# Kernel optimization log

Measured on AMD Instinct MI355X. Metric: run time of the kernel, lower is better.

Reference implementation:

```python
import jax, jax.numpy as jnp
import numpy as np

N, E, DIN, DH, NG, DOUT = 65536, 524288, 128, 128, 256, 3
EPS = 1e-5  # torch BatchNorm1d default


def setup_inputs():
    key = jax.random.key(0)
    ks = jax.random.split(key, 32)

    def p(k, shape, s=0.05):
        return jax.random.normal(k, shape, jnp.float32) * s

    inp = {
        "x": jax.random.normal(ks[0], (N, DIN), jnp.float32),
        "edge_index": jax.random.randint(ks[1], (2, E), 0, N),
        "batch": jnp.sort(jax.random.randint(ks[2], (N,), 0, NG)),
    }
    # live GATv2 layers: gat1 128->128, gat2 128->64, gat3 64->32 (gat4 output is
    # overwritten by h4 = dropout(h3) in the source, so gat4/m4 are dead code)
    dims = [(DIN, 128), (128, 64), (64, 32)]
    i = 3
    for l, (di, do) in enumerate(dims, start=1):
        inp[f"g{l}_Wl"] = p(ks[i], (di, do)); i += 1
        inp[f"g{l}_bl"] = jnp.zeros((do,), jnp.float32)
        inp[f"g{l}_Wr"] = p(ks[i], (di, do)); i += 1
        inp[f"g{l}_br"] = jnp.zeros((do,), jnp.float32)
        inp[f"g{l}_att"] = p(ks[i], (do,)); i += 1
        inp[f"g{l}_b"] = jnp.zeros((do,), jnp.float32)
        inp[f"bn{l}_g"] = jnp.ones((do,), jnp.float32)
        inp[f"bn{l}_b"] = jnp.zeros((do,), jnp.float32)
    inp["lin1_W"] = p(ks[i], (256, 128)); i += 1
    inp["lin1_b"] = jnp.zeros((128,), jnp.float32)
    inp["bn5_g"] = jnp.ones((128,), jnp.float32)
    inp["bn5_b"] = jnp.zeros((128,), jnp.float32)
    inp["lin2_W"] = p(ks[i], (128, DOUT)); i += 1
    inp["lin2_b"] = jnp.zeros((DOUT,), jnp.float32)
    inp["train"] = 0  # dropout disabled (eval)
    return inp


def _bn(h, g, b):
    # BatchNorm1d with batch statistics (biased variance, as torch normalizes)
    mu = h.mean(0)
    var = h.var(0)
    return g * (h - mu) * jax.lax.rsqrt(var + EPS) + b


def _gatv2(x, src, dst, Wl, bl, Wr, br, att, b, n):
    xl = x @ Wl + bl  # [N, C] source-side transform (also the message value)
    xr = x @ Wr + br  # [N, C] target-side transform
    e = jax.nn.leaky_relu(xl[src] + xr[dst], 0.2) @ att  # [E] attention logits
    m = jax.ops.segment_max(e, dst, num_segments=n)      # segment softmax over in-edges
    ex = jnp.exp(e - m[dst])
    alpha = ex / jax.ops.segment_sum(ex, dst, num_segments=n)[dst]
    return jax.ops.segment_sum(alpha[:, None] * xl[src], dst, num_segments=n) + b


def reference(x, edge_index, batch,
              g1_Wl, g1_bl, g1_Wr, g1_br, g1_att, g1_b, bn1_g, bn1_b,
              g2_Wl, g2_bl, g2_Wr, g2_br, g2_att, g2_b, bn2_g, bn2_b,
              g3_Wl, g3_bl, g3_Wr, g3_br, g3_att, g3_b, bn3_g, bn3_b,
              lin1_W, lin1_b, bn5_g, bn5_b, lin2_W, lin2_b, train):
    loops = jnp.arange(N)
    src = jnp.concatenate([edge_index[0], loops])  # PyG add_self_loops=True
    dst = jnp.concatenate([edge_index[1], loops])

    h1 = _bn(jax.nn.relu(_gatv2(x,  src, dst, g1_Wl, g1_bl, g1_Wr, g1_br, g1_att, g1_b, N)), bn1_g, bn1_b)
    h2 = _bn(jax.nn.relu(_gatv2(h1, src, dst, g2_Wl, g2_bl, g2_Wr, g2_br, g2_att, g2_b, N)), bn2_g, bn2_b)
    h3 = _bn(jax.nn.relu(_gatv2(h2, src, dst, g3_Wl, g3_bl, g3_Wr, g3_br, g3_att, g3_b, N)), bn3_g, bn3_b)

    p1 = jax.ops.segment_sum(h1, batch, num_segments=NG)  # global_add_pool
    p2 = jax.ops.segment_sum(h2, batch, num_segments=NG)
    p3 = jax.ops.segment_sum(h3, batch, num_segments=NG)
    # source overwrites h4 = dropout(h3), so the fourth pooled block is h3 again
    h = jnp.concatenate([p1, p2, p3, p3], axis=1)  # [NG, 256]

    h = _bn(jax.nn.relu(h @ lin1_W + lin1_b), bn5_g, bn5_b)
    h = h @ lin2_W + lin2_b
    return (jax.nn.sigmoid(h), jax.nn.log_softmax(h, axis=1))
```

## Files before the change

kernel.cpp:

```cpp
#include <hip/hip_runtime.h>
#include <math.h>
#include <type_traits>

#define NN 65536
#define NE 524288
#define NT (NN + NE)
#define NG 256
#define BN_EPS 1e-5f
#define NSLOT 64

typedef __attribute__((ext_vector_type(8))) __bf16 bf16x8;
typedef __attribute__((ext_vector_type(4))) float f32x4;

__device__ inline unsigned pk2(float lo, float hi) {
    unsigned a = (unsigned)__builtin_bit_cast(unsigned short, (__bf16)lo);
    unsigned b = (unsigned)__builtin_bit_cast(unsigned short, (__bf16)hi);
    return a | (b << 16);
}
__device__ inline void bf2(unsigned u, float& a, float& b) {
    a = __uint_as_float(u << 16);
    b = __uint_as_float(u & 0xFFFF0000u);
}
__device__ inline void unpk(uint4 u, float* v) {
    bf2(u.x, v[0], v[1]); bf2(u.y, v[2], v[3]);
    bf2(u.z, v[4], v[5]); bf2(u.w, v[6], v[7]);
}
__device__ inline void unpk(uint2 u, float* v) {
    bf2(u.x, v[0], v[1]); bf2(u.y, v[2], v[3]);
}
__device__ inline void unpk(unsigned u, float* v) { bf2(u, v[0], v[1]); }


__global__ void k_hist(const int* __restrict__ ei, int* __restrict__ counts) {
    int i = blockIdx.x * blockDim.x + threadIdx.x;
    if (i >= NE) return;
    atomicAdd(&counts[ei[NE + i]], 1);
}

__global__ void k_scanA(const int* __restrict__ counts, int* __restrict__ bsum) {
    __shared__ int l[256];
    int t = threadIdx.x;
    int v = counts[blockIdx.x * 256 + t] + 1;
    l[t] = v;
    __syncthreads();
    for (int st = 128; st > 0; st >>= 1) {
        if (t < st) l[t] += l[t + st];
        __syncthreads();
    }
    if (t == 0) bsum[blockIdx.x] = l[0];
}

__global__ void k_scanB(int* __restrict__ bsum, int* __restrict__ boff) {
    __shared__ int l[256];
    int t = threadIdx.x;
    int v = bsum[t];
    l[t] = v;
    __syncthreads();
    for (int d = 1; d < 256; d <<= 1) {
        int u = (t >= d) ? l[t - d] : 0;
        __syncthreads();
        l[t] += u;
        __syncthreads();
    }
    boff[t] = l[t] - v;
}

__global__ void k_scanC(const int* __restrict__ counts, const int* __restrict__ boff,
                        int* __restrict__ off, int* __restrict__ wofs) {
    __shared__ int l[256];
    int t = threadIdx.x;
    int i = blockIdx.x * 256 + t;
    int v = counts[i] + 1;
    l[t] = v;
    __syncthreads();
    for (int d = 1; d < 256; d <<= 1) {
        int u = (t >= d) ? l[t - d] : 0;
        __syncthreads();
        l[t] += u;
        __syncthreads();
    }
    int e = boff[blockIdx.x] + l[t] - v;
    off[i] = e;
    wofs[i] = e;
    if (i == 0) off[NN] = NT;
}


__global__ void k_scatter(const int* __restrict__ ei, const int* __restrict__ batch,
                          int* __restrict__ wofs, int* __restrict__ csr_src,
                          int* __restrict__ gstart, int* __restrict__ gend) {
    int i = blockIdx.x * blockDim.x + threadIdx.x;
    if (i >= NT) return;
    if (i < NN) {
        int b = batch[i];
        if (i == 0) gstart[b] = 0;
        if (i == NN - 1) gend[b] = NN;
        else {
            int b2 = batch[i + 1];
            if (b2 != b) { gend[b] = i + 1; gstart[b2] = i + 1; }
        }
    }
    int src, dst;
    if (i < NE) { src = ei[i]; dst = ei[NE + i]; }
    else        { src = dst = i - NE; }
    int pos = atomicAdd(&wofs[dst], 1);
    csr_src[pos] = src;
}


__global__ void k_wswz_all(const float* __restrict__ W1l, const float* __restrict__ W1r,
                           const float* __restrict__ W2l, const float* __restrict__ W2r,
                           const float* __restrict__ W3l, const float* __restrict__ W3r,
                           unsigned short* __restrict__ f1l, unsigned short* __restrict__ f1r,
                           unsigned short* __restrict__ f2l, unsigned short* __restrict__ f2r,
                           unsigned short* __restrict__ f3l, unsigned short* __restrict__ f3r) {
    int idx = blockIdx.x * 256 + threadIdx.x;
    const float* W; unsigned short* Wf; int DO, base;
    if (idx < 2048)      { W = W1l; Wf = f1l; DO = 128; base = 0; }
    else if (idx < 4096) { W = W1r; Wf = f1r; DO = 128; base = 2048; }
    else if (idx < 5120) { W = W2l; Wf = f2l; DO = 64;  base = 4096; }
    else if (idx < 6144) { W = W2r; Wf = f2r; DO = 64;  base = 5120; }
    else if (idx < 6400) { W = W3l; Wf = f3l; DO = 32;  base = 6144; }
    else if (idx < 6656) { W = W3r; Wf = f3r; DO = 32;  base = 6400; }
    else return;
    int li = idx - base;
    int lane = li & 63;
    int fr = li >> 6;
    int nf = fr % (DO / 16);
    int kk = fr / (DO / 16);
    int k0 = kk * 32 + (lane >> 4) * 8;
    int c = nf * 16 + (lane & 15);
    unsigned short o[8];
#pragma unroll
    for (int j = 0; j < 8; ++j)
        o[j] = __builtin_bit_cast(unsigned short, (__bf16)W[(size_t)(k0 + j) * DO + c]);
    uint4 p;
    p.x = o[0] | ((unsigned)o[1] << 16);
    p.y = o[2] | ((unsigned)o[3] << 16);
    p.z = o[4] | ((unsigned)o[5] << 16);
    p.w = o[6] | ((unsigned)o[7] << 16);
    ((uint4*)(Wf))[li] = p;
}


template <int DI, int DO, bool BN>
__global__ __launch_bounds__(256) void k_gemm2m(
        const float* __restrict__ x,
        const unsigned short* __restrict__ Wfl, const unsigned short* __restrict__ Wfr,
        const float* __restrict__ bl, const float* __restrict__ br,
        const float* __restrict__ stats, const float* __restrict__ bg,
        const float* __restrict__ bb,
        unsigned short* __restrict__ xl, unsigned short* __restrict__ xr) {
    constexpr int NF = DO / 16;
    constexpr int NK = DI / 32;
    const int lane = threadIdx.x & 63;
    const int wid = threadIdx.x >> 6;
    const int lg = lane >> 4, ll = lane & 15;
    const int nbase = blockIdx.x * 128 + wid * 32;

    __shared__ float ssc[DI], ssh[DI];
    if constexpr (BN) {
        int t = threadIdx.x;
        if (t < DI) {
            float s = 0.f, q = 0.f;
            for (int k = 0; k < NSLOT; ++k) {
                s += stats[k * 2 * DI + t];
                q += stats[k * 2 * DI + DI + t];
            }
            float mean = s * (1.f / NN);
            float var = q * (1.f / NN) - mean * mean;
            float sc = bg[t] * rsqrtf(var + BN_EPS);
            ssc[t] = sc;
            ssh[t] = bb[t] - mean * sc;
        }
        __syncthreads();
    }

    f32x4 acc[2][NF][2] = {};

    for (int kk = 0; kk < NK; ++kk) {
        const int k0 = kk * 32 + lg * 8;
        float4 sca, scb, sha, shb;
        if constexpr (BN) {
            sca = *(const float4*)(ssc + k0);
            scb = *(const float4*)(ssc + k0 + 4);
            sha = *(const float4*)(ssh + k0);
            shb = *(const float4*)(ssh + k0 + 4);
        }
        bf16x8 xa[2];
#pragma unroll
        for (int nm = 0; nm < 2; ++nm) {
            const float* xp = x + (size_t)(nbase + nm * 16 + ll) * DI + k0;
            float4 v0 = *(const float4*)xp;
            float4 v1 = *(const float4*)(xp + 4);
            if constexpr (BN) {
                v0.x = v0.x * sca.x + sha.x;
                v0.y = v0.y * sca.y + sha.y;
                v0.z = v0.z * sca.z + sha.z;
                v0.w = v0.w * sca.w + sha.w;
                v1.x = v1.x * scb.x + shb.x;
                v1.y = v1.y * scb.y + shb.y;
                v1.z = v1.z * scb.z + shb.z;
                v1.w = v1.w * scb.w + shb.w;
            }
            bf16x8 t;
            t[0] = (__bf16)v0.x; t[1] = (__bf16)v0.y;
            t[2] = (__bf16)v0.z; t[3] = (__bf16)v0.w;
            t[4] = (__bf16)v1.x; t[5] = (__bf16)v1.y;
            t[6] = (__bf16)v1.z; t[7] = (__bf16)v1.w;
            xa[nm] = t;
        }
        const unsigned short* wlp = Wfl + ((size_t)(kk * NF) * 64 + lane) * 8;
        const unsigned short* wrp = Wfr + ((size_t)(kk * NF) * 64 + lane) * 8;
#pragma unroll
        for (int nf = 0; nf < NF; ++nf) {
            bf16x8 wl = __builtin_bit_cast(bf16x8, *(const uint4*)(wlp + (size_t)nf * 64 * 8));
            bf16x8 wr = __builtin_bit_cast(bf16x8, *(const uint4*)(wrp + (size_t)nf * 64 * 8));
#pragma unroll
            for (int nm = 0; nm < 2; ++nm) {
                acc[nm][nf][0] = __builtin_amdgcn_mfma_f32_16x16x32_bf16(wl, xa[nm], acc[nm][nf][0], 0, 0, 0);
                acc[nm][nf][1] = __builtin_amdgcn_mfma_f32_16x16x32_bf16(wr, xa[nm], acc[nm][nf][1], 0, 0, 0);
            }
        }
    }

#pragma unroll
    for (int nf = 0; nf < NF; ++nf) {
        float4 blv = *(const float4*)(bl + nf * 16 + lg * 4);
        float4 brv = *(const float4*)(br + nf * 16 + lg * 4);
#pragma unroll
        for (int nm = 0; nm < 2; ++nm) {
            size_t base = (size_t)(nbase + nm * 16 + ll) * DO + nf * 16 + lg * 4;
            f32x4 a = acc[nm][nf][0];
            uint2 p;
            p.x = pk2(a[0] + blv.x, a[1] + blv.y);
            p.y = pk2(a[2] + blv.z, a[3] + blv.w);
            *(uint2*)(xl + base) = p;
            f32x4 r = acc[nm][nf][1];
            uint2 q;
            q.x = pk2(r[0] + brv.x, r[1] + brv.y);
            q.y = pk2(r[2] + brv.z, r[3] + brv.w);
            *(uint2*)(xr + base) = q;
        }
    }
}


template <int DO, bool WRITEH, int PBASE>
__global__ __launch_bounds__(256) void k_agg7(
        const unsigned short* __restrict__ xl, const unsigned short* __restrict__ xr,
        const int* __restrict__ off, const int* __restrict__ srcs,
        const float* __restrict__ att, const float* __restrict__ bias,
        const int* __restrict__ batch,
        float* __restrict__ out, float* __restrict__ statbuf,
        float* __restrict__ rawpool) {
    constexpr int CPL = DO / 16;
    using UT = typename std::conditional<CPL == 8, uint4,
               typename std::conditional<CPL == 4, uint2, unsigned>::type>::type;
    int wid = threadIdx.x >> 6;
    int lane = threadIdx.x & 63;
    int sg = lane >> 4;
    int sl = lane & 15;
    int node = blockIdx.x * 4 + wid;
    int cbase = sl * CPL;

    __shared__ float sO[4][DO];
    __shared__ int sgb[4];
    if (threadIdx.x < 4) sgb[threadIdx.x] = batch[blockIdx.x * 4 + threadIdx.x];

    float xrv[CPL], atv[CPL];
    unpk(*(const UT*)(xr + (size_t)node * DO + cbase), xrv);
    if constexpr (CPL == 8) {
        float4 a0 = ((const float4*)att)[sl * 2], a1 = ((const float4*)att)[sl * 2 + 1];
        atv[0] = a0.x; atv[1] = a0.y; atv[2] = a0.z; atv[3] = a0.w;
        atv[4] = a1.x; atv[5] = a1.y; atv[6] = a1.z; atv[7] = a1.w;
    } else if constexpr (CPL == 4) {
        float4 a0 = ((const float4*)att)[sl];
        atv[0] = a0.x; atv[1] = a0.y; atv[2] = a0.z; atv[3] = a0.w;
    } else {
        float2 a0 = ((const float2*)att)[sl];
        atv[0] = a0.x; atv[1] = a0.y;
    }

    float spart = 0.f;
    float acc[CPL] = {};
    int e0 = off[node], e1 = off[node + 1];

    int jp = e0 + sg;
    bool actp = (jp < e1);
    int srcp = srcs[actp ? jp : e1 - 1];
    UT up = *(const UT*)(xl + (size_t)srcp * DO + cbase);

    for (int jb = e0; jb < e1; jb += 4) {
        UT u = up;
        bool act = actp;
        if (jb + 4 < e1) {
            int jn = jb + 4 + sg;
            actp = (jn < e1);
            int srcn = srcs[actp ? jn : e1 - 1];
            up = *(const UT*)(xl + (size_t)srcn * DO + cbase);
        }
        float v[CPL];
        unpk(u, v);
        float pd = 0.f;
#pragma unroll
        for (int i = 0; i < CPL; ++i) {
            float t = v[i] + xrv[i];
            t = fmaxf(t, 0.2f * t);
            pd = fmaf(t, atv[i], pd);
        }
#pragma unroll
        for (int d = 1; d < 16; d <<= 1) pd += __shfl_xor(pd, d);
        float w = act ? __expf(pd) : 0.f;
        spart += w;
#pragma unroll
        for (int i = 0; i < CPL; ++i) acc[i] = fmaf(w, v[i], acc[i]);
    }
    spart += __shfl_xor(spart, 16);
    spart += __shfl_xor(spart, 32);
#pragma unroll
    for (int i = 0; i < CPL; ++i) {
        acc[i] += __shfl_xor(acc[i], 16);
        acc[i] += __shfl_xor(acc[i], 32);
    }
    if (sg == 0) {
        float inv = 1.f / spart;
        float o[CPL];
#pragma unroll
        for (int i = 0; i < CPL; ++i) {
            o[i] = fmaxf(acc[i] * inv + bias[cbase + i], 0.f);
            sO[wid][cbase + i] = o[i];
        }
        if constexpr (WRITEH) {
            if constexpr (CPL == 8) {
                float4 oa = {o[0], o[1], o[2], o[3]}, ob = {o[4], o[5], o[6], o[7]};
                ((float4*)out)[(size_t)node * 32 + sl * 2] = oa;
                ((float4*)out)[(size_t)node * 32 + sl * 2 + 1] = ob;
            } else if constexpr (CPL == 4) {
                float4 oa = {o[0], o[1], o[2], o[3]};
                ((float4*)out)[(size_t)node * 16 + sl] = oa;
            } else {
                float2 oa = {o[0], o[1]};
                ((float2*)out)[(size_t)node * 16 + sl] = oa;
            }
        }
    }
    __syncthreads();
    int t = threadIdx.x;
    if (t < DO) {
        float v0 = sO[0][t], v1 = sO[1][t], v2 = sO[2][t], v3 = sO[3][t];
        float* sb = statbuf + (size_t)(blockIdx.x & (NSLOT - 1)) * 2 * DO;
        atomicAdd(&sb[t], v0 + v1 + v2 + v3);
        atomicAdd(&sb[DO + t], v0 * v0 + v1 * v1 + v2 * v2 + v3 * v3);
        float pa = v0;
        int cg = sgb[0];
        float vv[3] = {v1, v2, v3};
#pragma unroll
        for (int w = 1; w < 4; ++w) {
            int g = sgb[w];
            if (g != cg) {
                atomicAdd(&rawpool[(size_t)cg * 224 + PBASE + t], pa);
                pa = 0.f;
                cg = g;
            }
            pa += vv[w - 1];
        }
        atomicAdd(&rawpool[(size_t)cg * 224 + PBASE + t], pa);
    }
}


__global__ __launch_bounds__(128) void k_head1(
        const float* __restrict__ rawpool,
        const int* __restrict__ gstart, const int* __restrict__ gend,
        const float* __restrict__ st1, const float* __restrict__ st2,
        const float* __restrict__ st3,
        const float* __restrict__ g1, const float* __restrict__ b1,
        const float* __restrict__ g2, const float* __restrict__ b2,
        const float* __restrict__ g3, const float* __restrict__ b3,
        const float* __restrict__ W1, const float* __restrict__ b1l,
        float* __restrict__ z) {
    __shared__ float row[256];
    int g = blockIdx.x, c = threadIdx.x;
    float cnt = (float)(gend[g] - gstart[g]);
    {
        float s = 0.f, q = 0.f;
        for (int k = 0; k < NSLOT; ++k) {
            s += st1[k * 256 + c];
            q += st1[k * 256 + 128 + c];
        }
        float mean = s * (1.f / NN);
        float var = q * (1.f / NN) - mean * mean;
        float sc = g1[c] * rsqrtf(var + BN_EPS);
        float sh = b1[c] - mean * sc;
        row[c] = sc * rawpool[(size_t)g * 224 + c] + sh * cnt;
    }
    {
        float sc, sh, rv;
        if (c < 64) {
            float s = 0.f, q = 0.f;
            for (int k = 0; k < NSLOT; ++k) {
                s += st2[k * 128 + c];
                q += st2[k * 128 + 64 + c];
            }
            float mean = s * (1.f / NN);
            float var = q * (1.f / NN) - mean * mean;
            sc = g2[c] * rsqrtf(var + BN_EPS);
            sh = b2[c] - mean * sc;
            rv = rawpool[(size_t)g * 224 + 128 + c];
        } else {
            int j = (c < 96) ? c - 64 : c - 96;
            float s = 0.f, q = 0.f;
            for (int k = 0; k < NSLOT; ++k) {
                s += st3[k * 64 + j];
                q += st3[k * 64 + 32 + j];
            }
            float mean = s * (1.f / NN);
            float var = q * (1.f / NN) - mean * mean;
            sc = g3[j] * rsqrtf(var + BN_EPS);
            sh = b3[j] - mean * sc;
            rv = rawpool[(size_t)g * 224 + 192 + j];
        }
        row[128 + c] = sc * rv + sh * cnt;
    }
    __syncthreads();
    float acc = b1l[c];
#pragma unroll 16
    for (int k = 0; k < 256; ++k) acc += row[k] * W1[k * 128 + c];
    z[g * 128 + c] = acc > 0.f ? acc : 0.f;
}

__global__ void k_head2(const float* __restrict__ z, const float* __restrict__ g5,
                        const float* __restrict__ b5, const float* __restrict__ W2,
                        const float* __restrict__ b2, float* __restrict__ out) {
    __shared__ float row[128];
    __shared__ float lg[3];
    int g = blockIdx.x, t = threadIdx.x;
    double s = 0.0, q = 0.0;
    for (int gg = 0; gg < NG; ++gg) {
        float v = z[gg * 128 + t];
        s += v;
        q += (double)v * v;
    }
    double mean = s * (1.0 / NG);
    double var = q * (1.0 / NG) - mean * mean;
    float sc = g5[t] * rsqrtf((float)var + BN_EPS);
    float sh = b5[t] - (float)mean * sc;
    row[t] = z[g * 128 + t] * sc + sh;
    __syncthreads();
    if (t < 3) {
        float acc = b2[t];
        for (int k = 0; k < 128; ++k) acc += row[k] * W2[k * 3 + t];
        lg[t] = acc;
    }
    __syncthreads();
    if (t == 0) {
        float l0 = lg[0], l1 = lg[1], l2 = lg[2];
        float mx = fmaxf(l0, fmaxf(l1, l2));
        float lse = mx + logf(expf(l0 - mx) + expf(l1 - mx) + expf(l2 - mx));
        out[g * 3 + 0] = 1.f / (1.f + expf(-l0));
        out[g * 3 + 1] = 1.f / (1.f + expf(-l1));
        out[g * 3 + 2] = 1.f / (1.f + expf(-l2));
        out[NG * 3 + g * 3 + 0] = l0 - lse;
        out[NG * 3 + g * 3 + 1] = l1 - lse;
        out[NG * 3 + g * 3 + 2] = l2 - lse;
    }
}


extern "C" void kernel_launch(void* const* d_in, const int* in_sizes, int n_in,
                              void* d_out, int out_size, void* d_ws, size_t ws_size,
                              hipStream_t stream) {
    const float* x   = (const float*)d_in[0];
    const int* ei    = (const int*)d_in[1];
    const int* batch = (const int*)d_in[2];
    auto F = [&](int i) { return (const float*)d_in[i]; };

    char* ws = (char*)d_ws;
    size_t o = 0;
    auto alloc = [&](size_t bytes) {
        char* p = ws + o;
        o += (bytes + 255) & ~(size_t)255;
        return p;
    };
    int* csr_off  = (int*)alloc((NN + 1) * 4);
    int* counts   = (int*)alloc(NN * 4);
    int* wofs     = (int*)alloc(NN * 4);
    int* bsum     = (int*)alloc(256 * 4);
    int* boff     = (int*)alloc(256 * 4);
    int* csr_src  = (int*)alloc((size_t)NT * 4);
    unsigned short* xl = (unsigned short*)alloc((size_t)NN * 128 * 2);
    unsigned short* xr = (unsigned short*)alloc((size_t)NN * 128 * 2);
    float* h1     = (float*)alloc((size_t)NN * 128 * 4);
    float* h2     = (float*)alloc((size_t)NN * 64 * 4);
    float* z      = (float*)alloc(NG * 128 * 4);
    size_t zbytes = (size_t)NSLOT * (256 + 128 + 64) * 4 + (size_t)NG * 224 * 4 + 2 * NG * 4;
    char* zchunk  = alloc(zbytes);
    float* stat1  = (float*)zchunk;
    float* stat2  = stat1 + NSLOT * 256;
    float* stat3  = stat2 + NSLOT * 128;
    float* rawpool = stat3 + NSLOT * 64;
    int* gstart   = (int*)(rawpool + (size_t)NG * 224);
    int* gend     = gstart + NG;
    unsigned short* wfl1 = (unsigned short*)alloc(128 * 128 * 2);
    unsigned short* wfr1 = (unsigned short*)alloc(128 * 128 * 2);
    unsigned short* wfl2 = (unsigned short*)alloc(128 * 64 * 2);
    unsigned short* wfr2 = (unsigned short*)alloc(128 * 64 * 2);
    unsigned short* wfl3 = (unsigned short*)alloc(64 * 32 * 2);
    unsigned short* wfr3 = (unsigned short*)alloc(64 * 32 * 2);

    hipMemsetAsync(counts, 0, NN * 4, stream);
    hipMemsetAsync(zchunk, 0, zbytes, stream);
    k_hist<<<(NE + 255) / 256, 256, 0, stream>>>(ei, counts);
    k_scanA<<<NN / 256, 256, 0, stream>>>(counts, bsum);
    k_scanB<<<1, 256, 0, stream>>>(bsum, boff);
    k_scanC<<<NN / 256, 256, 0, stream>>>(counts, boff, csr_off, wofs);
    k_scatter<<<(NT + 255) / 256, 256, 0, stream>>>(ei, batch, wofs, csr_src,
                                                    gstart, gend);
    k_wswz_all<<<26, 256, 0, stream>>>(F(3), F(5), F(11), F(13), F(19), F(21),
                                       wfl1, wfr1, wfl2, wfr2, wfl3, wfr3);

    k_gemm2m<128, 128, false><<<NN / 128, 256, 0, stream>>>(
        x, wfl1, wfr1, F(4), F(6), nullptr, nullptr, nullptr, xl, xr);
    k_agg7<128, true, 0><<<NN / 4, 256, 0, stream>>>(
        xl, xr, csr_off, csr_src, F(7), F(8), batch, h1, stat1, rawpool);

    k_gemm2m<128, 64, true><<<NN / 128, 256, 0, stream>>>(
        h1, wfl2, wfr2, F(12), F(14), stat1, F(9), F(10), xl, xr);
    k_agg7<64, true, 128><<<NN / 4, 256, 0, stream>>>(
        xl, xr, csr_off, csr_src, F(15), F(16), batch, h2, stat2, rawpool);

    k_gemm2m<64, 32, true><<<NN / 128, 256, 0, stream>>>(
        h2, wfl3, wfr3, F(20), F(22), stat2, F(17), F(18), xl, xr);
    k_agg7<32, false, 192><<<NN / 4, 256, 0, stream>>>(
        xl, xr, csr_off, csr_src, F(23), F(24), batch, nullptr, stat3, rawpool);

    k_head1<<<NG, 128, 0, stream>>>(rawpool, gstart, gend, stat1, stat2, stat3,
                                    F(9), F(10), F(17), F(18), F(25), F(26),
                                    F(27), F(28), z);
    k_head2<<<NG, 128, 0, stream>>>(z, F(29), F(30), F(31), F(32), (float*)d_out);
}
```

Before: 274.6 us.

## Merge preprocessing kernels and process 16 nodes per aggregation block

Folds the histogram and weight swizzle into one launch and merges the two scan-offset kernels into one. Runs the CSR scatter and the first-layer GEMM in a single heterogeneous launch, and drops a separate memset by moving counts into the zeroed chunk. The aggregation kernel now handles 16 nodes per block (4 per wave) instead of 4, which cuts the number of stat and pool atomics per node. This trades fewer launches and less atomic traffic for lower block-level parallelism in aggregation and redundant block-prefix scans in each scan block.

```diff
diff --git a/kernel.cpp b/kernel.cpp
--- a/kernel.cpp
+++ b/kernel.cpp
@@ -31,98 +31,27 @@
 __device__ inline void unpk(unsigned u, float* v) { bf2(u, v[0], v[1]); }
 
 
-__global__ void k_hist(const int* __restrict__ ei, int* __restrict__ counts) {
-    int i = blockIdx.x * blockDim.x + threadIdx.x;
-    if (i >= NE) return;
-    atomicAdd(&counts[ei[NE + i]], 1);
-}
-
-__global__ void k_scanA(const int* __restrict__ counts, int* __restrict__ bsum) {
-    __shared__ int l[256];
-    int t = threadIdx.x;
-    int v = counts[blockIdx.x * 256 + t] + 1;
-    l[t] = v;
-    __syncthreads();
-    for (int st = 128; st > 0; st >>= 1) {
-        if (t < st) l[t] += l[t + st];
-        __syncthreads();
-    }
-    if (t == 0) bsum[blockIdx.x] = l[0];
-}
-
-__global__ void k_scanB(int* __restrict__ bsum, int* __restrict__ boff) {
-    __shared__ int l[256];
-    int t = threadIdx.x;
-    int v = bsum[t];
-    l[t] = v;
-    __syncthreads();
-    for (int d = 1; d < 256; d <<= 1) {
-        int u = (t >= d) ? l[t - d] : 0;
-        __syncthreads();
-        l[t] += u;
-        __syncthreads();
-    }
-    boff[t] = l[t] - v;
-}
-
-__global__ void k_scanC(const int* __restrict__ counts, const int* __restrict__ boff,
-                        int* __restrict__ off, int* __restrict__ wofs) {
-    __shared__ int l[256];
-    int t = threadIdx.x;
-    int i = blockIdx.x * 256 + t;
-    int v = counts[i] + 1;
-    l[t] = v;
-    __syncthreads();
-    for (int d = 1; d < 256; d <<= 1) {
-        int u = (t >= d) ? l[t - d] : 0;
-        __syncthreads();
-        l[t] += u;
-        __syncthreads();
-    }
-    int e = boff[blockIdx.x] + l[t] - v;
-    off[i] = e;
-    wofs[i] = e;
-    if (i == 0) off[NN] = NT;
-}
-
-
-__global__ void k_scatter(const int* __restrict__ ei, const int* __restrict__ batch,
-                          int* __restrict__ wofs, int* __restrict__ csr_src,
-                          int* __restrict__ gstart, int* __restrict__ gend) {
-    int i = blockIdx.x * blockDim.x + threadIdx.x;
-    if (i >= NT) return;
-    if (i < NN) {
-        int b = batch[i];
-        if (i == 0) gstart[b] = 0;
-        if (i == NN - 1) gend[b] = NN;
-        else {
-            int b2 = batch[i + 1];
-            if (b2 != b) { gend[b] = i + 1; gstart[b2] = i + 1; }
-        }
-    }
-    int src, dst;
-    if (i < NE) { src = ei[i]; dst = ei[NE + i]; }
-    else        { src = dst = i - NE; }
-    int pos = atomicAdd(&wofs[dst], 1);
-    csr_src[pos] = src;
-}
-
-
-__global__ void k_wswz_all(const float* __restrict__ W1l, const float* __restrict__ W1r,
-                           const float* __restrict__ W2l, const float* __restrict__ W2r,
-                           const float* __restrict__ W3l, const float* __restrict__ W3r,
-                           unsigned short* __restrict__ f1l, unsigned short* __restrict__ f1r,
-                           unsigned short* __restrict__ f2l, unsigned short* __restrict__ f2r,
-                           unsigned short* __restrict__ f3l, unsigned short* __restrict__ f3r) {
-    int idx = blockIdx.x * 256 + threadIdx.x;
+__global__ __launch_bounds__(256) void k_pre(
+        const int* __restrict__ ei, int* __restrict__ counts,
+        const float* __restrict__ W1l, const float* __restrict__ W1r,
+        const float* __restrict__ W2l, const float* __restrict__ W2r,
+        const float* __restrict__ W3l, const float* __restrict__ W3r,
+        unsigned short* __restrict__ f1l, unsigned short* __restrict__ f1r,
+        unsigned short* __restrict__ f2l, unsigned short* __restrict__ f2r,
+        unsigned short* __restrict__ f3l, unsigned short* __restrict__ f3r) {
+    if (blockIdx.x < 2048) {
+        int i = blockIdx.x * 256 + threadIdx.x;
+        atomicAdd(&counts[ei[NE + i]], 1);
+        return;
+    }
+    int idx = (blockIdx.x - 2048) * 256 + threadIdx.x;
     const float* W; unsigned short* Wf; int DO, base;
     if (idx < 2048)      { W = W1l; Wf = f1l; DO = 128; base = 0; }
     else if (idx < 4096) { W = W1r; Wf = f1r; DO = 128; base = 2048; }
     else if (idx < 5120) { W = W2l; Wf = f2l; DO = 64;  base = 4096; }
     else if (idx < 6144) { W = W2r; Wf = f2r; DO = 64;  base = 5120; }
     else if (idx < 6400) { W = W3l; Wf = f3l; DO = 32;  base = 6144; }
-    else if (idx < 6656) { W = W3r; Wf = f3r; DO = 32;  base = 6400; }
-    else return;
+    else                 { W = W3r; Wf = f3r; DO = 32;  base = 6400; }
     int li = idx - base;
     int lane = li & 63;
     int fr = li >> 6;
@@ -143,9 +72,55 @@
 }
 
 
+__global__ void k_scanA(const int* __restrict__ counts, int* __restrict__ bsum) {
+    __shared__ int l[256];
+    int t = threadIdx.x;
+    int v = counts[blockIdx.x * 256 + t] + 1;
+    l[t] = v;
+    __syncthreads();
+    for (int st = 128; st > 0; st >>= 1) {
+        if (t < st) l[t] += l[t + st];
+        __syncthreads();
+    }
+    if (t == 0) bsum[blockIdx.x] = l[0];
+}
+
+
+__global__ void k_scanBC(const int* __restrict__ counts, const int* __restrict__ bsum,
+                         int* __restrict__ off, int* __restrict__ wofs) {
+    __shared__ int lb[256];
+    __shared__ int l[256];
+    int t = threadIdx.x;
+    int bv = bsum[t];
+    lb[t] = bv;
+    __syncthreads();
+    for (int d = 1; d < 256; d <<= 1) {
+        int u = (t >= d) ? lb[t - d] : 0;
+        __syncthreads();
+        lb[t] += u;
+        __syncthreads();
+    }
+    int boffv = lb[blockIdx.x] - bsum[blockIdx.x];
+    int i = blockIdx.x * 256 + t;
+    int v = counts[i] + 1;
+    l[t] = v;
+    __syncthreads();
+    for (int d = 1; d < 256; d <<= 1) {
+        int u = (t >= d) ? l[t - d] : 0;
+        __syncthreads();
+        l[t] += u;
+        __syncthreads();
+    }
+    int e = boffv + l[t] - v;
+    off[i] = e;
+    wofs[i] = e;
+    if (i == 0) off[NN] = NT;
+}
+
+
 template <int DI, int DO, bool BN>
-__global__ __launch_bounds__(256) void k_gemm2m(
-        const float* __restrict__ x,
+__device__ void gemm2m_body(
+        int bid, const float* __restrict__ x,
         const unsigned short* __restrict__ Wfl, const unsigned short* __restrict__ Wfr,
         const float* __restrict__ bl, const float* __restrict__ br,
         const float* __restrict__ stats, const float* __restrict__ bg,
@@ -156,9 +131,11 @@
     const int lane = threadIdx.x & 63;
     const int wid = threadIdx.x >> 6;
     const int lg = lane >> 4, ll = lane & 15;
-    const int nbase = blockIdx.x * 128 + wid * 32;
-
-    __shared__ float ssc[DI], ssh[DI];
+    const int nbase = bid * 128 + wid * 32;
+
+    __shared__ float sbn[BN ? 2 * DI : 2];
+    float* ssc = sbn;
+    float* ssh = sbn + (BN ? DI : 1);
     if constexpr (BN) {
         int t = threadIdx.x;
         if (t < DI) {
@@ -245,9 +222,51 @@
     }
 }
 
+template <int DI, int DO, bool BN>
+__global__ __launch_bounds__(256) void k_gemm2m(
+        const float* __restrict__ x,
+        const unsigned short* __restrict__ Wfl, const unsigned short* __restrict__ Wfr,
+        const float* __restrict__ bl, const float* __restrict__ br,
+        const float* __restrict__ stats, const float* __restrict__ bg,
+        const float* __restrict__ bb,
+        unsigned short* __restrict__ xl, unsigned short* __restrict__ xr) {
+    gemm2m_body<DI, DO, BN>(blockIdx.x, x, Wfl, Wfr, bl, br, stats, bg, bb, xl, xr);
+}
+
+
+__global__ __launch_bounds__(256) void k_scatgem(
+        const int* __restrict__ ei, const int* __restrict__ batch,
+        int* __restrict__ wofs, int* __restrict__ csr_src,
+        int* __restrict__ gstart, int* __restrict__ gend,
+        const float* __restrict__ x,
+        const unsigned short* __restrict__ wfl1, const unsigned short* __restrict__ wfr1,
+        const float* __restrict__ bl, const float* __restrict__ br,
+        unsigned short* __restrict__ xl, unsigned short* __restrict__ xr) {
+    if (blockIdx.x < NT / 256) {
+        int i = blockIdx.x * 256 + threadIdx.x;
+        if (i < NN) {
+            int b = batch[i];
+            if (i == 0) gstart[b] = 0;
+            if (i == NN - 1) gend[b] = NN;
+            else {
+                int b2 = batch[i + 1];
+                if (b2 != b) { gend[b] = i + 1; gstart[b2] = i + 1; }
+            }
+        }
+        int src, dst;
+        if (i < NE) { src = ei[i]; dst = ei[NE + i]; }
+        else        { src = dst = i - NE; }
+        int pos = atomicAdd(&wofs[dst], 1);
+        csr_src[pos] = src;
+        return;
+    }
+    gemm2m_body<128, 128, false>(blockIdx.x - NT / 256, x, wfl1, wfr1, bl, br,
+                                 nullptr, nullptr, nullptr, xl, xr);
+}
+
 
 template <int DO, bool WRITEH, int PBASE>
-__global__ __launch_bounds__(256) void k_agg7(
+__global__ __launch_bounds__(256) void k_agg8(
         const unsigned short* __restrict__ xl, const unsigned short* __restrict__ xr,
         const int* __restrict__ off, const int* __restrict__ srcs,
         const float* __restrict__ att, const float* __restrict__ bias,
@@ -261,15 +280,13 @@
     int lane = threadIdx.x & 63;
     int sg = lane >> 4;
     int sl = lane & 15;
-    int node = blockIdx.x * 4 + wid;
     int cbase = sl * CPL;
 
-    __shared__ float sO[4][DO];
-    __shared__ int sgb[4];
-    if (threadIdx.x < 4) sgb[threadIdx.x] = batch[blockIdx.x * 4 + threadIdx.x];
-
-    float xrv[CPL], atv[CPL];
-    unpk(*(const UT*)(xr + (size_t)node * DO + cbase), xrv);
+    __shared__ float sO[16][DO];
+    __shared__ int gb[16];
+    if (threadIdx.x < 16) gb[threadIdx.x] = batch[blockIdx.x * 16 + threadIdx.x];
+
+    float atv[CPL];
     if constexpr (CPL == 8) {
         float4 a0 = ((const float4*)att)[sl * 2], a1 = ((const float4*)att)[sl * 2 + 1];
         atv[0] = a0.x; atv[1] = a0.y; atv[2] = a0.z; atv[3] = a0.w;
@@ -282,90 +299,98 @@
         atv[0] = a0.x; atv[1] = a0.y;
     }
 
-    float spart = 0.f;
-    float acc[CPL] = {};
-    int e0 = off[node], e1 = off[node + 1];
-
-    int jp = e0 + sg;
-    bool actp = (jp < e1);
-    int srcp = srcs[actp ? jp : e1 - 1];
-    UT up = *(const UT*)(xl + (size_t)srcp * DO + cbase);
-
-    for (int jb = e0; jb < e1; jb += 4) {
-        UT u = up;
-        bool act = actp;
-        if (jb + 4 < e1) {
-            int jn = jb + 4 + sg;
-            actp = (jn < e1);
-            int srcn = srcs[actp ? jn : e1 - 1];
-            up = *(const UT*)(xl + (size_t)srcn * DO + cbase);
-        }
-        float v[CPL];
-        unpk(u, v);
-        float pd = 0.f;
+    int nb = blockIdx.x * 16 + wid * 4;
+    for (int n = 0; n < 4; ++n) {
+        int node = nb + n;
+        float xrv[CPL];
+        unpk(*(const UT*)(xr + (size_t)node * DO + cbase), xrv);
+        float spart = 0.f;
+        float acc[CPL] = {};
+        int e0 = off[node], e1 = off[node + 1];
+
+        int jp = e0 + sg;
+        bool actp = (jp < e1);
+        int srcp = srcs[actp ? jp : e1 - 1];
+        UT up = *(const UT*)(xl + (size_t)srcp * DO + cbase);
+
+        for (int jb = e0; jb < e1; jb += 4) {
+            UT u = up;
+            bool act = actp;
+            if (jb + 4 < e1) {
+                int jn = jb + 4 + sg;
+                actp = (jn < e1);
+                int srcn = srcs[actp ? jn : e1 - 1];
+                up = *(const UT*)(xl + (size_t)srcn * DO + cbase);
+            }
+            float v[CPL];
+            unpk(u, v);
+            float pd = 0.f;
+#pragma unroll
+            for (int i = 0; i < CPL; ++i) {
+                float t = v[i] + xrv[i];
+                t = fmaxf(t, 0.2f * t);
+                pd = fmaf(t, atv[i], pd);
+            }
+#pragma unroll
+            for (int d = 1; d < 16; d <<= 1) pd += __shfl_xor(pd, d);
+            float w = act ? __expf(pd) : 0.f;
+            spart += w;
+#pragma unroll
+            for (int i = 0; i < CPL; ++i) acc[i] = fmaf(w, v[i], acc[i]);
+        }
+        spart += __shfl_xor(spart, 16);
+        spart += __shfl_xor(spart, 32);
 #pragma unroll
         for (int i = 0; i < CPL; ++i) {
-            float t = v[i] + xrv[i];
-            t = fmaxf(t, 0.2f * t);
-            pd = fmaf(t, atv[i], pd);
-        }
-#pragma unroll
-        for (int d = 1; d < 16; d <<= 1) pd += __shfl_xor(pd, d);
-        float w = act ? __expf(pd) : 0.f;
-        spart += w;
-#pragma unroll
-        for (int i = 0; i < CPL; ++i) acc[i] = fmaf(w, v[i], acc[i]);
-    }
-    spart += __shfl_xor(spart, 16);
-    spart += __shfl_xor(spart, 32);
-#pragma unroll
-    for (int i = 0; i < CPL; ++i) {
-        acc[i] += __shfl_xor(acc[i], 16);
-        acc[i] += __shfl_xor(acc[i], 32);
-    }
-    if (sg == 0) {
-        float inv = 1.f / spart;
-        float o[CPL];
-#pragma unroll
-        for (int i = 0; i < CPL; ++i) {
-            o[i] = fmaxf(acc[i] * inv + bias[cbase + i], 0.f);
-            sO[wid][cbase + i] = o[i];
-        }
-        if constexpr (WRITEH) {
-            if constexpr (CPL == 8) {
-                float4 oa = {o[0], o[1], o[2], o[3]}, ob = {o[4], o[5], o[6], o[7]};
-                ((float4*)out)[(size_t)node * 32 + sl * 2] = oa;
-                ((float4*)out)[(size_t)node * 32 + sl * 2 + 1] = ob;
-            } else if constexpr (CPL == 4) {
-                float4 oa = {o[0], o[1], o[2], o[3]};
-                ((float4*)out)[(size_t)node * 16 + sl] = oa;
-            } else {
-                float2 oa = {o[0], o[1]};
-                ((float2*)out)[(size_t)node * 16 + sl] = oa;
+            acc[i] += __shfl_xor(acc[i], 16);
+            acc[i] += __shfl_xor(acc[i], 32);
+        }
+        if (sg == 0) {
+            float inv = 1.f / spart;
+            float o[CPL];
+#pragma unroll
+            for (int i = 0; i < CPL; ++i) {
+                o[i] = fmaxf(acc[i] * inv + bias[cbase + i], 0.f);
+                sO[wid * 4 + n][cbase + i] = o[i];
+            }
+            if constexpr (WRITEH) {
+                if constexpr (CPL == 8) {
+                    float4 oa = {o[0], o[1], o[2], o[3]}, ob = {o[4], o[5], o[6], o[7]};
+                    ((float4*)out)[(size_t)node * 32 + sl * 2] = oa;
+                    ((float4*)out)[(size_t)node * 32 + sl * 2 + 1] = ob;
+                } else if constexpr (CPL == 4) {
+                    float4 oa = {o[0], o[1], o[2], o[3]};
+                    ((float4*)out)[(size_t)node * 16 + sl] = oa;
+                } else {
+                    float2 oa = {o[0], o[1]};
+                    ((float2*)out)[(size_t)node * 16 + sl] = oa;
+                }
             }
         }
     }
     __syncthreads();
     int t = threadIdx.x;
     if (t < DO) {
-        float v0 = sO[0][t], v1 = sO[1][t], v2 = sO[2][t], v3 = sO[3][t];
-        float* sb = statbuf + (size_t)(blockIdx.x & (NSLOT - 1)) * 2 * DO;
-        atomicAdd(&sb[t], v0 + v1 + v2 + v3);
-        atomicAdd(&sb[DO + t], v0 * v0 + v1 * v1 + v2 * v2 + v3 * v3);
-        float pa = v0;
-        int cg = sgb[0];
-        float vv[3] = {v1, v2, v3};
-#pragma unroll
-        for (int w = 1; w < 4; ++w) {
-            int g = sgb[w];
+        float pa = sO[0][t];
+        float s = pa, q = pa * pa;
+        int cg = gb[0];
+#pragma unroll
+        for (int w = 1; w < 16; ++w) {
+            float vw = sO[w][t];
+            s += vw;
+            q += vw * vw;
+            int g = gb[w];
             if (g != cg) {
                 atomicAdd(&rawpool[(size_t)cg * 224 + PBASE + t], pa);
                 pa = 0.f;
                 cg = g;
             }
-            pa += vv[w - 1];
+            pa += vw;
         }
         atomicAdd(&rawpool[(size_t)cg * 224 + PBASE + t], pa);
+        float* sb = statbuf + (size_t)(blockIdx.x & (NSLOT - 1)) * 2 * DO;
+        atomicAdd(&sb[t], s);
+        atomicAdd(&sb[DO + t], q);
     }
 }
 
@@ -484,19 +509,19 @@
         return p;
     };
     int* csr_off  = (int*)alloc((NN + 1) * 4);
-    int* counts   = (int*)alloc(NN * 4);
     int* wofs     = (int*)alloc(NN * 4);
     int* bsum     = (int*)alloc(256 * 4);
-    int* boff     = (int*)alloc(256 * 4);
     int* csr_src  = (int*)alloc((size_t)NT * 4);
     unsigned short* xl = (unsigned short*)alloc((size_t)NN * 128 * 2);
     unsigned short* xr = (unsigned short*)alloc((size_t)NN * 128 * 2);
     float* h1     = (float*)alloc((size_t)NN * 128 * 4);
     float* h2     = (float*)alloc((size_t)NN * 64 * 4);
     float* z      = (float*)alloc(NG * 128 * 4);
-    size_t zbytes = (size_t)NSLOT * (256 + 128 + 64) * 4 + (size_t)NG * 224 * 4 + 2 * NG * 4;
+    size_t zbytes = (size_t)NN * 4 + (size_t)NSLOT * (256 + 128 + 64) * 4 +
+                    (size_t)NG * 224 * 4 + 2 * NG * 4;
     char* zchunk  = alloc(zbytes);
-    float* stat1  = (float*)zchunk;
+    int* counts   = (int*)zchunk;
+    float* stat1  = (float*)(zchunk + (size_t)NN * 4);
     float* stat2  = stat1 + NSLOT * 256;
     float* stat3  = stat2 + NSLOT * 128;
     float* rawpool = stat3 + NSLOT * 64;
@@ -509,30 +534,28 @@
     unsigned short* wfl3 = (unsigned short*)alloc(64 * 32 * 2);
     unsigned short* wfr3 = (unsigned short*)alloc(64 * 32 * 2);
 
-    hipMemsetAsync(counts, 0, NN * 4, stream);
     hipMemsetAsync(zchunk, 0, zbytes, stream);
-    k_hist<<<(NE + 255) / 256, 256, 0, stream>>>(ei, counts);
+
+    k_pre<<<2048 + 26, 256, 0, stream>>>(ei, counts,
+                                         F(3), F(5), F(11), F(13), F(19), F(21),
+                                         wfl1, wfr1, wfl2, wfr2, wfl3, wfr3);
     k_scanA<<<NN / 256, 256, 0, stream>>>(counts, bsum);
-    k_scanB<<<1, 256, 0, stream>>>(bsum, boff);
-    k_scanC<<<NN / 256, 256, 0, stream>>>(counts, boff, csr_off, wofs);
-    k_scatter<<<(NT + 255) / 256, 256, 0, stream>>>(ei, batch, wofs, csr_src,
-                                                    gstart, gend);
-    k_wswz_all<<<26, 256, 0, stream>>>(F(3), F(5), F(11), F(13), F(19), F(21),
-                                       wfl1, wfr1, wfl2, wfr2, wfl3, wfr3);
-
-    k_gemm2m<128, 128, false><<<NN / 128, 256, 0, stream>>>(
-        x, wfl1, wfr1, F(4), F(6), nullptr, nullptr, nullptr, xl, xr);
-    k_agg7<128, true, 0><<<NN / 4, 256, 0, stream>>>(
+    k_scanBC<<<NN / 256, 256, 0, stream>>>(counts, bsum, csr_off, wofs);
+
+    k_scatgem<<<NT / 256 + NN / 128, 256, 0, stream>>>(
+        ei, batch, wofs, csr_src, gstart, gend,
+        x, wfl1, wfr1, F(4), F(6), xl, xr);
+    k_agg8<128, true, 0><<<NN / 16, 256, 0, stream>>>(
         xl, xr, csr_off, csr_src, F(7), F(8), batch, h1, stat1, rawpool);
 
     k_gemm2m<128, 64, true><<<NN / 128, 256, 0, stream>>>(
         h1, wfl2, wfr2, F(12), F(14), stat1, F(9), F(10), xl, xr);
-    k_agg7<64, true, 128><<<NN / 4, 256, 0, stream>>>(
+    k_agg8<64, true, 128><<<NN / 16, 256, 0, stream>>>(
         xl, xr, csr_off, csr_src, F(15), F(16), batch, h2, stat2, rawpool);
 
     k_gemm2m<64, 32, true><<<NN / 128, 256, 0, stream>>>(
         h2, wfl3, wfr3, F(20), F(22), stat2, F(17), F(18), xl, xr);
-    k_agg7<32, false, 192><<<NN / 4, 256, 0, stream>>>(
+    k_agg8<32, false, 192><<<NN / 16, 256, 0, stream>>>(
         xl, xr, csr_off, csr_src, F(23), F(24), batch, nullptr, stat3, rawpool);
 
     k_head1<<<NG, 128, 0, stream>>>(rawpool, gstart, gend, stat1, stat2, stat3,
```

After: 246.1 us. -10.4%, faster.
